# Kernel optimization log

Hardware: AMD Instinct MI355X
Metric: run time of the kernel (lower is better)

Reference implementation:

```python
import jax, jax.numpy as jnp
import numpy as np

# ---- geometry constants (match init_kwargs) ----
A = 24            # standardAngleNum
U, V = 128, 64    # detectorSize = [U, V]
W, H, D = 128, 128, 64  # volumeSize = [W, H, D]
SID, SDD = 256.0, 512.0
S = 128           # samples per ray
HS = 100.0        # half-span of ray sampling around isocenter (covers volume half-diagonal ~96)
STEP = 2.0 * HS / S
ANGLES = np.deg2rad(np.linspace(0.0, 360.0, A, False)).astype(np.float32)
LAMB = 1.0


def _cos_weight():
    # cosine[..., i, j] = SDD / sqrt(SDD^2 + (i - V/2)^2 + (j - U/2)^2), i over V, j over U
    i = np.arange(V)[:, None].astype(np.float64)
    j = np.arange(U)[None, :].astype(np.float64)
    w = SDD / np.sqrt(SDD ** 2 + (i - V / 2.0) ** 2 + (j - U / 2.0) ** 2)
    return jnp.asarray(w[None, None, None], jnp.float32)  # [1,1,1,V,U], broadcasts over A


def _ramp():
    # Ram-Lak spatial-domain filter, length U+1, OIHW kernel [1,1,1,U+1]
    i = np.arange(U + 1, dtype=np.float64)
    mid = np.floor(U / 2.0)
    d = i - mid
    f = np.where(d % 2 == 0, 0.0, -0.5 / (np.pi ** 2 * np.where(d == 0, 1.0, d * d)))
    f[int(mid)] = 0.125  # 1/8 at center
    return jnp.asarray(f.reshape(1, 1, 1, U + 1), jnp.float32)


COSW = _cos_weight()
RAMP = _ramp()


def forward_project(vol):
    """Ray-driven cone-beam forward projection. vol: [D,H,W] -> sino [A,V,U]. Linear in vol."""
    uu = jnp.arange(U, dtype=jnp.float32) - (U - 1) / 2.0
    vv = jnp.arange(V, dtype=jnp.float32) - (V - 1) / 2.0
    ell = jnp.linspace(SID - HS, SID + HS, S, dtype=jnp.float32)  # distance from source

    def body(_, cs):
        c, s = cs
        z = jnp.zeros_like(c)
        src = jnp.stack([-SID * c, -SID * s, z])                 # source position [3]
        dc = jnp.stack([(SDD - SID) * c, (SDD - SID) * s, z])    # detector center [3]
        uax = jnp.stack([-s, c, z])                              # detector u axis
        vax = jnp.array([0.0, 0.0, 1.0], jnp.float32)            # detector v axis
        pix = dc + uu[None, :, None] * uax + vv[:, None, None] * vax  # [V,U,3]
        dirs = pix - src
        dirs = dirs / jnp.linalg.norm(dirs, axis=-1, keepdims=True)   # unit ray dirs [V,U,3]
        pts = src + ell[:, None, None, None] * dirs[None]             # [S,V,U,3]
        coords = [pts[..., 2] + (D - 1) / 2.0,   # z -> depth index
                  pts[..., 1] + (H - 1) / 2.0,   # y -> row index
                  pts[..., 0] + (W - 1) / 2.0]   # x -> col index
        vals = jax.scipy.ndimage.map_coordinates(vol, coords, order=1, mode='constant', cval=0.0)
        return None, vals.sum(axis=0) * STEP     # [V,U]

    ang = jnp.asarray(ANGLES)
    _, sino = jax.lax.scan(body, None, (jnp.cos(ang), jnp.sin(ang)))
    return sino  # [A,V,U]


def back_project(sino):
    """Exact adjoint of forward_project (matches projector.forward/backward adjoint pair)."""
    _, vjp = jax.vjp(forward_project, jnp.zeros((D, H, W), jnp.float32))
    (vol,) = vjp(sino)
    return vol


def fbp(x, p):
    # residual = FP(x) - p
    sino = forward_project(x[0, 0])[None, None]       # [1,1,A,V,U]
    res = (sino - p) * COSW                           # cosine weighting
    # ramp filtering along detector u, done as conv2d on [b,c,A*V,U]
    r2 = res.reshape(1, 1, A * V, U)
    r2 = jax.lax.conv_general_dilated(r2, RAMP, (1, 1), ((0, 0), (U // 2, U // 2)),
                                      dimension_numbers=('NCHW', 'OIHW', 'NCHW'))
    res = r2.reshape(1, 1, A, V, U)
    return LAMB * back_project(res[0, 0])[None, None]  # [1,1,D,H,W]


def setup_inputs() -> dict:
    key = jax.random.key(0)
    k1, k2 = jax.random.split(key)
    x = jax.random.normal(k1, (1, 1, D, H, W), jnp.float32)
    p = jax.random.normal(k2, (1, 1, A, V, U), jnp.float32)
    return {"x": x, "p": p}


def reference(x, p):
    return fbp(x, p)
```

## Files before the change

kernel.cpp:

```cpp
#include <hip/hip_runtime.h>
#include <math.h>

#define NA   24
#define NU   128
#define NV   64
#define NW   128
#define NH   128
#define ND   64
#define NS   128
#define F_STEP 1.5625f
#define F_DL  (200.0f / 127.0f)
#define F_L0  156.0f
#define INV_DL (127.0f / 200.0f)

#define NRAYS (NA * NV * NU)
#define VOX   (NW * NH * ND)
#define NSEG  4

#define PPX  130
#define PPY  130
#define PPZ  68
#define PPLANE (PPX * PPY)
#define PVN  (PPZ * PPLANE)
#define CBASE (2 * PPLANE + PPX + 1)

typedef float v2f __attribute__((ext_vector_type(2)));

__device__ __constant__ float CSA[NA] = {
    1.0f,  0.96592582628906829f,  0.86602540378443865f,  0.70710678118654752f,
    0.5f,  0.25881904510252076f,  0.0f,                 -0.25881904510252076f,
   -0.5f, -0.70710678118654752f, -0.86602540378443865f, -0.96592582628906829f,
   -1.0f, -0.96592582628906829f, -0.86602540378443865f, -0.70710678118654752f,
   -0.5f, -0.25881904510252076f,  0.0f,                  0.25881904510252076f,
    0.5f,  0.70710678118654752f,  0.86602540378443865f,  0.96592582628906829f
};
__device__ __constant__ float SNA[NA] = {
    0.0f,  0.25881904510252076f,  0.5f,                  0.70710678118654752f,
    0.86602540378443865f,  0.96592582628906829f,  1.0f,  0.96592582628906829f,
    0.86602540378443865f,  0.70710678118654752f,  0.5f,  0.25881904510252076f,
    0.0f, -0.25881904510252076f, -0.5f,                 -0.70710678118654752f,
   -0.86602540378443865f, -0.96592582628906829f, -1.0f, -0.96592582628906829f,
   -0.86602540378443865f, -0.70710678118654752f, -0.5f, -0.25881904510252076f
};

__global__ __launch_bounds__(256) void pad_kernel(const float* __restrict__ vol,
                                                  float* __restrict__ padv) {
    int i = blockIdx.x * 256 + threadIdx.x;
    if (i >= PVN) return;
    int x = i % PPX;
    int t = i / PPX;
    int y = t % PPY;
    int z = t / PPY;
    float val = 0.0f;
    if (z >= 2 && z <= 65 && y >= 1 && y <= 128 && x >= 1 && x <= 128)
        val = vol[(((z - 2) << 7) + (y - 1) << 7) + (x - 1)];
    padv[i] = val;
}

__device__ __forceinline__ void ray_setup(int a, int v, int u,
                                          float& sx, float& sy,
                                          float& dx, float& dy, float& dz) {
    float ang = (float)((double)a * (15.0 * M_PI / 180.0));
    float c = cosf(ang), s = sinf(ang);
    float uu = (float)u - 63.5f;
    float vv = (float)v - 31.5f;
    float ux = 512.0f * c - uu * s;
    float uy = 512.0f * s + uu * c;
    float uz = vv;
    float invn = 1.0f / sqrtf(ux * ux + uy * uy + uz * uz);
    dx = ux * invn; dy = uy * invn; dz = uz * invn;
    sx = -256.0f * c; sy = -256.0f * s;
}

__global__ __launch_bounds__(256) void fp_seg_kernel(const float* __restrict__ padv,
                                                     float* __restrict__ part) {
    int r = blockIdx.x * blockDim.x + threadIdx.x;
    int seg = blockIdx.y;
    int u = r & (NU - 1);
    int v = (r >> 7) & (NV - 1);
    int a = r >> 13;

    float sx, sy, dx, dy, dz;
    ray_setup(a, v, u, sx, sy, dx, dy, dz);

    float rx = 1.0f / dx, ry = 1.0f / dy, rz = 1.0f / dz;
    float ex0 = (-64.51f - sx) * rx, ex1 = (64.51f - sx) * rx;
    float ey0 = (-64.51f - sy) * ry, ey1 = (64.51f - sy) * ry;
    float ez0 = (-32.51f) * rz,      ez1 = (32.51f) * rz;
    float llo = fmaxf(fmaxf(fminf(ex0, ex1), fminf(ey0, ey1)), fminf(ez0, ez1));
    float lhi = fminf(fminf(fmaxf(ex0, ex1), fmaxf(ey0, ey1)), fmaxf(ez0, ez1));
    int i_lo = max(seg * 32,      (int)ceilf((llo - F_L0) * INV_DL));
    int i_hi = min(seg * 32 + 31, (int)floorf((lhi - F_L0) * INV_DL));

    float acc = 0.0f;
    for (int i = i_lo; i <= i_hi; ++i) {
        float ell = fmaf((float)i, F_DL, F_L0);
        float cx = fmaf(ell, dx, sx) + 63.5f;
        float cy = fmaf(ell, dy, sy) + 63.5f;
        float cz = ell * dz + 31.5f;
        float fx = floorf(cx), fy = floorf(cy), fz = floorf(cz);
        int ix = (int)fx, iy = (int)fy, iz = (int)fz;
        float wx1 = cx - fx, wy1 = cy - fy, wz1 = cz - fz;
        int base = iz * PPLANE + iy * PPX + ix + CBASE;
        const float* q0 = padv + base;
        const float* q1 = q0 + PPLANE;
        float v000 = q0[0],   v001 = q0[1];
        float v010 = q0[PPX], v011 = q0[PPX + 1];
        float v100 = q1[0],   v101 = q1[1];
        float v110 = q1[PPX], v111 = q1[PPX + 1];
        float c00 = fmaf(wx1, v001 - v000, v000);
        float c01 = fmaf(wx1, v011 - v010, v010);
        float c10 = fmaf(wx1, v101 - v100, v100);
        float c11 = fmaf(wx1, v111 - v110, v110);
        float c0  = fmaf(wy1, c01 - c00, c00);
        float c1  = fmaf(wy1, c11 - c10, c10);
        acc += fmaf(wz1, c1 - c0, c0);
    }
    part[seg * NRAYS + r] = acc;
}

__global__ __launch_bounds__(NU) void ramp_kernel(const float* __restrict__ part,
                                                  const float* __restrict__ p,
                                                  float* __restrict__ resT) {
    __shared__ float row[NU];
    int rowid = blockIdx.x;
    int u = threadIdx.x;
    int e = rowid * NU + u;
    int a = rowid >> 6;
    int v = rowid & (NV - 1);
    float sino = (part[e] + part[NRAYS + e] + part[2 * NRAYS + e] + part[3 * NRAYS + e]) * F_STEP;
    double du = (double)u - 64.0;
    double dv = (double)v - 32.0;
    float cw = (float)(512.0 / sqrt(262144.0 + dv * dv + du * du));
    row[u] = (sino - p[e]) * cw;
    __syncthreads();
    float acc = 0.125f * row[u];
#pragma unroll
    for (int d = 1; d <= 63; d += 2) {
        float f = (float)(-0.5 / (M_PI * M_PI * (double)(d * d)));
        float lo = (u - d >= 0) ? row[u - d] : 0.0f;
        float hi = (u + d < NU) ? row[u + d] : 0.0f;
        acc += f * (lo + hi);
    }
    resT[(a << 13) + (u << 6) + v] = acc;
}


#define SETUP_ANGLE(S, AIDX, AB)                                                 \
    const float c##S = CSA[AIDX], sn##S = SNA[AIDX];                             \
    const float c512##S = 512.0f * c##S;                                         \
    const float s512##S = 512.0f * sn##S;                                        \
    const float rho##S = fmaf(x0, c##S, fmaf(y0, sn##S, 256.0f));                \
    const float Vx##S = x0 + 256.0f * c##S;                                      \
    const float Vy##S = y0 + 256.0f * sn##S;                                     \
    const float tvlo##S = (rho##S - (AB)) * (1.0f / 512.0f);                     \
    const float yp##S = y0 * c##S - x0 * sn##S;                                  \
    const float rl##S = __builtin_amdgcn_rcpf(rho##S - (AB));                    \
    const float rh##S = __builtin_amdgcn_rcpf(rho##S + (AB));                    \
    const float A##S = yp##S - (AB), B##S = yp##S + (AB);                        \
    const float um##S = 512.0f * A##S * ((A##S >= 0.0f) ? rh##S : rl##S);        \
    const float uM##S = 512.0f * B##S * ((B##S >= 0.0f) ? rl##S : rh##S);        \
    const int u_lo##S = max(0,   (int)ceilf(um##S + 63.49f));                    \
    const int u_hi##S = min(127, (int)floorf(uM##S + 63.51f));                   \
    const int len##S = max(0, u_hi##S - u_lo##S + 1);                            \
    const float Zmin##S = fmaf(vvf, (vvf >= 0.0f) ? (tvlo##S - 1.0e-3f)          \
                                                  : (tvlo##S + 7.2e-3f), 31.5f); \
    const float izbf##S = floorf(Zmin##S);                                       \
    const int   izb##S  = (int)izbf##S;                                          \
    const v2f b0##S = {izbf##S, izbf##S};                                        \
    const float tDL##S = tvlo##S * INV_DL;                                       \
    const v2f mVx##S = {-Vx##S, -Vx##S}, mVy##S = {-Vy##S, -Vy##S};

#define BP_BODY2(S, RV, UU) do {                                                 \
    const float pu = fmaf(-(UU), sn##S, c512##S);                                \
    const float qu = fmaf((UU), c##S, s512##S);                                  \
    const float arg  = fmaf((UU), (UU), s2);                                     \
    const float invn = __builtin_amdgcn_rsqf(arg);                               \
    const float nn   = arg * invn;                                               \
    const float i0f  = ceilf(fmaf(tDL##S, nn, cK));                              \
    const float ell0 = fmaf(i0f, F_DL, F_L0);                                    \
    v2f tp; tp.x = ell0 * invn; tp.y = fmaf(F_DL, invn, tp.x);                   \
    const v2f pu2 = {pu, pu}, qu2 = {qu, qu};                                    \
    v2f wx = __builtin_elementwise_max(                                          \
        one2 - __builtin_elementwise_abs(__builtin_elementwise_fma(tp, pu2, mVx##S)), zero2); \
    v2f wy = __builtin_elementwise_max(                                          \
        one2 - __builtin_elementwise_abs(__builtin_elementwise_fma(tp, qu2, mVy##S)), zero2); \
    v2f val = wx * wy * (v2f){(RV), (RV)};                                       \
    const v2f fz2 = __builtin_elementwise_fma(tp, vv2, h31);                     \
    const v2f g = fz2 - b0##S;                                                   \
    AC0##S = __builtin_elementwise_fma(__builtin_elementwise_max(                \
             one2 - __builtin_elementwise_abs(g), zero2), val, AC0##S);          \
    AC1##S = __builtin_elementwise_fma(__builtin_elementwise_max(                \
             one2 - __builtin_elementwise_abs(g - one2), zero2), val, AC1##S);   \
    AC2##S = __builtin_elementwise_fma(__builtin_elementwise_max(                \
             one2 - __builtin_elementwise_abs(g - two2), zero2), val, AC2##S);   \
} while (0)

__global__ __launch_bounds__(256, 8) void bp_gather14(const float* __restrict__ resT,
                                                      float* __restrict__ out) {
    __shared__ float s_acc[4 * 64];

    const int tid  = threadIdx.x;
    const int lane = tid & 63;
    const int wv   = tid >> 6;
    const int y    = blockIdx.x & 127;
    const int xq   = blockIdx.x >> 7;
    const int xi   = xq * 4 + wv;

    const float x0 = (float)xi - 63.5f;
    const float y0 = (float)y  - 63.5f;
    const float vvf = (float)lane - 31.5f;
    const float s2  = fmaf(vvf, vvf, 262144.0f);
    const v2f vv2   = {vvf, vvf};
    const v2f one2  = {1.0f, 1.0f}, zero2 = {0.0f, 0.0f};
    const v2f two2  = {2.0f, 2.0f};
    const v2f h31   = {31.5f, 31.5f};
    const float cK  = -(F_L0 * INV_DL) - 1.0e-3f;

    s_acc[tid] = 0.0f;

    for (int j = 0; j < NA / 2; ++j) {
        const int a0 = 2 * j, a1 = 2 * j + 1;
        const float ab1a = fabsf(CSA[a0]) + fabsf(SNA[a0]);
        const float ab1b = fabsf(CSA[a1]) + fabsf(SNA[a1]);

        SETUP_ANGLE(0, a0, ab1a);
        SETUP_ANGLE(1, a1, ab1b);

        const int trips = (max(len0, len1) + 1) & ~1;
        if (trips == 0) continue;
        const int us0 = max(0, min(u_lo0, 128 - trips));
        const int us1 = max(0, min(u_lo1, 128 - trips));

        v2f AC00 = zero2, AC10 = zero2, AC20 = zero2;
        v2f AC01 = zero2, AC11 = zero2, AC21 = zero2;

        const float* ru0 = resT + (a0 << 13) + (us0 << 6) + lane;
        const float* ru1 = resT + (a1 << 13) + (us1 << 6) + lane;
        float uu0 = (float)us0 - 63.5f;
        float uu1 = (float)us1 - 63.5f;

        float Ar0 = ru0[0],  Ar1 = ru1[0];
        float Br0 = ru0[64], Br1 = ru1[64];
#pragma unroll 1
        for (int k = 0; k < trips; k += 2) {
            const float Cr0 = ru0[128];
            const float Cr1 = ru1[128];
            const float Dr0 = ru0[192];
            const float Dr1 = ru1[192];
            BP_BODY2(0, Ar0, uu0);
            BP_BODY2(1, Ar1, uu1);
            BP_BODY2(0, Br0, uu0 + 1.0f);
            BP_BODY2(1, Br1, uu1 + 1.0f);
            Ar0 = Cr0; Ar1 = Cr1; Br0 = Dr0; Br1 = Dr1;
            ru0 += 128; ru1 += 128;
            uu0 += 2.0f; uu1 += 2.0f;
        }

        float* accw = s_acc + (wv << 6);
        atomicAdd(&accw[izb0],     AC00.x + AC00.y);
        atomicAdd(&accw[izb0 + 1], AC10.x + AC10.y);
        atomicAdd(&accw[izb0 + 2], AC20.x + AC20.y);
        atomicAdd(&accw[izb1],     AC01.x + AC01.y);
        atomicAdd(&accw[izb1 + 1], AC11.x + AC11.y);
        atomicAdd(&accw[izb1 + 2], AC21.x + AC21.y);
    }
    __syncthreads();

    const int z  = tid >> 2;
    const int w4 = tid & 3;
    out[(z << 14) + (y << 7) + xq * 4 + w4] = s_acc[(w4 << 6) + z] * F_STEP;
}

extern "C" void kernel_launch(void* const* d_in, const int* in_sizes, int n_in,
                              void* d_out, int out_size, void* d_ws, size_t ws_size,
                              hipStream_t stream) {
    const float* x = (const float*)d_in[0];
    const float* p = (const float*)d_in[1];
    float* out  = (float*)d_out;
    float* resT = (float*)d_ws;
    float* part = resT + NRAYS;
    float* padv = part + NSEG * NRAYS;

    pad_kernel<<<(PVN + 255) / 256, 256, 0, stream>>>(x, padv);
    dim3 fpg(NRAYS / 256, NSEG);
    fp_seg_kernel<<<fpg, 256, 0, stream>>>(padv, part);
    ramp_kernel<<<NA * NV, NU, 0, stream>>>(part, p, resT);
    bp_gather14<<<128 * 32, 256, 0, stream>>>(resT, out);
}
```

Baseline: 431.3 us.

## Software-pipeline angle-pair setup and first loads in backprojection gather

Computes the geometry and issues the first two residual loads for the next angle pair before processing the current pair, so setup latency and load latency overlap the inner accumulation loop. It also simplifies the third z-weight to max(g-2+1,0) form (max(h1,0)) and relaxes launch bounds from 8 to 4 blocks per SM, giving more registers at the cost of potential occupancy. The zero-trip early skip is removed, and the last iteration prefetches pair 0 redundantly.

```diff
diff --git a/kernel.cpp b/kernel.cpp
--- a/kernel.cpp
+++ b/kernel.cpp
@@ -146,57 +146,73 @@
 }
 
 
-#define SETUP_ANGLE(S, AIDX, AB)                                                 \
-    const float c##S = CSA[AIDX], sn##S = SNA[AIDX];                             \
-    const float c512##S = 512.0f * c##S;                                         \
-    const float s512##S = 512.0f * sn##S;                                        \
-    const float rho##S = fmaf(x0, c##S, fmaf(y0, sn##S, 256.0f));                \
-    const float Vx##S = x0 + 256.0f * c##S;                                      \
-    const float Vy##S = y0 + 256.0f * sn##S;                                     \
-    const float tvlo##S = (rho##S - (AB)) * (1.0f / 512.0f);                     \
-    const float yp##S = y0 * c##S - x0 * sn##S;                                  \
-    const float rl##S = __builtin_amdgcn_rcpf(rho##S - (AB));                    \
-    const float rh##S = __builtin_amdgcn_rcpf(rho##S + (AB));                    \
-    const float A##S = yp##S - (AB), B##S = yp##S + (AB);                        \
-    const float um##S = 512.0f * A##S * ((A##S >= 0.0f) ? rh##S : rl##S);        \
-    const float uM##S = 512.0f * B##S * ((B##S >= 0.0f) ? rl##S : rh##S);        \
-    const int u_lo##S = max(0,   (int)ceilf(um##S + 63.49f));                    \
-    const int u_hi##S = min(127, (int)floorf(uM##S + 63.51f));                   \
-    const int len##S = max(0, u_hi##S - u_lo##S + 1);                            \
-    const float Zmin##S = fmaf(vvf, (vvf >= 0.0f) ? (tvlo##S - 1.0e-3f)          \
-                                                  : (tvlo##S + 7.2e-3f), 31.5f); \
-    const float izbf##S = floorf(Zmin##S);                                       \
-    const int   izb##S  = (int)izbf##S;                                          \
-    const v2f b0##S = {izbf##S, izbf##S};                                        \
-    const float tDL##S = tvlo##S * INV_DL;                                       \
-    const v2f mVx##S = {-Vx##S, -Vx##S}, mVy##S = {-Vy##S, -Vy##S};
+#define DECL_ANG(P) \
+    float P##_c, P##_sn, P##_tDL, P##_izbf; \
+    int P##_ulo, P##_len, P##_us; \
+    float P##_Ar, P##_Br;
+
+#define COPY_ANG(D, S) do { \
+    D##_c = S##_c; D##_sn = S##_sn; D##_tDL = S##_tDL; D##_izbf = S##_izbf; \
+    D##_us = S##_us; D##_Ar = S##_Ar; D##_Br = S##_Br; \
+} while (0)
+
+#define SETUP_P(P, AIDX) do { \
+    const float c_ = CSA[(AIDX)], s_ = SNA[(AIDX)]; \
+    const float ab_ = fabsf(c_) + fabsf(s_); \
+    const float rho_ = fmaf(x0, c_, fmaf(y0, s_, 256.0f)); \
+    const float tvlo_ = (rho_ - ab_) * (1.0f / 512.0f); \
+    const float yp_ = y0 * c_ - x0 * s_; \
+    const float rl_ = __builtin_amdgcn_rcpf(rho_ - ab_); \
+    const float rh_ = __builtin_amdgcn_rcpf(rho_ + ab_); \
+    const float A_ = yp_ - ab_, B_ = yp_ + ab_; \
+    const float um_ = 512.0f * A_ * ((A_ >= 0.0f) ? rh_ : rl_); \
+    const float uM_ = 512.0f * B_ * ((B_ >= 0.0f) ? rl_ : rh_); \
+    P##_ulo = max(0, (int)ceilf(um_ + 63.49f)); \
+    P##_len = min(127, (int)floorf(uM_ + 63.51f)) - P##_ulo + 1; \
+    const float zm_ = fmaf(vvf, (vvf >= 0.0f) ? (tvlo_ - 1.0e-3f) \
+                                              : (tvlo_ + 7.2e-3f), 31.5f); \
+    P##_izbf = floorf(zm_); \
+    P##_tDL  = tvlo_ * INV_DL; \
+    P##_c = c_; P##_sn = s_; \
+} while (0)
+
+#define PAIR_FINISH(P0, P1, TR) do { \
+    TR = (max(max(P0##_len, P1##_len), 0) + 1) & ~1; \
+    P0##_us = max(0, min(P0##_ulo, 128 - TR)); \
+    P1##_us = max(0, min(P1##_ulo, 128 - TR)); \
+} while (0)
+
+#define ISSUE(P, AIDX) do { \
+    const float* r_ = resT + ((AIDX) << 13) + (P##_us << 6) + lane; \
+    P##_Ar = r_[0]; P##_Br = r_[64]; \
+} while (0)
 
 #define BP_BODY2(S, RV, UU) do {                                                 \
-    const float pu = fmaf(-(UU), sn##S, c512##S);                                \
-    const float qu = fmaf((UU), c##S, s512##S);                                  \
+    const float pu = fmaf(-(UU), ksn##S, kc512##S);                              \
+    const float qu = fmaf((UU), kc##S, ks512##S);                                \
     const float arg  = fmaf((UU), (UU), s2);                                     \
     const float invn = __builtin_amdgcn_rsqf(arg);                               \
     const float nn   = arg * invn;                                               \
-    const float i0f  = ceilf(fmaf(tDL##S, nn, cK));                              \
+    const float i0f  = ceilf(fmaf(ktDL##S, nn, cK));                             \
     const float ell0 = fmaf(i0f, F_DL, F_L0);                                    \
     v2f tp; tp.x = ell0 * invn; tp.y = fmaf(F_DL, invn, tp.x);                   \
     const v2f pu2 = {pu, pu}, qu2 = {qu, qu};                                    \
     v2f wx = __builtin_elementwise_max(                                          \
-        one2 - __builtin_elementwise_abs(__builtin_elementwise_fma(tp, pu2, mVx##S)), zero2); \
+        one2 - __builtin_elementwise_abs(__builtin_elementwise_fma(tp, pu2, kmVx##S)), zero2); \
     v2f wy = __builtin_elementwise_max(                                          \
-        one2 - __builtin_elementwise_abs(__builtin_elementwise_fma(tp, qu2, mVy##S)), zero2); \
+        one2 - __builtin_elementwise_abs(__builtin_elementwise_fma(tp, qu2, kmVy##S)), zero2); \
     v2f val = wx * wy * (v2f){(RV), (RV)};                                       \
     const v2f fz2 = __builtin_elementwise_fma(tp, vv2, h31);                     \
-    const v2f g = fz2 - b0##S;                                                   \
+    const v2f g  = fz2 - kb0##S;                                                 \
+    const v2f h1 = g - one2;                                                     \
     AC0##S = __builtin_elementwise_fma(__builtin_elementwise_max(                \
              one2 - __builtin_elementwise_abs(g), zero2), val, AC0##S);          \
     AC1##S = __builtin_elementwise_fma(__builtin_elementwise_max(                \
-             one2 - __builtin_elementwise_abs(g - one2), zero2), val, AC1##S);   \
-    AC2##S = __builtin_elementwise_fma(__builtin_elementwise_max(                \
-             one2 - __builtin_elementwise_abs(g - two2), zero2), val, AC2##S);   \
-} while (0)
-
-__global__ __launch_bounds__(256, 8) void bp_gather14(const float* __restrict__ resT,
+             one2 - __builtin_elementwise_abs(h1), zero2), val, AC1##S);         \
+    AC2##S = __builtin_elementwise_fma(__builtin_elementwise_max(h1, zero2), val, AC2##S); \
+} while (0)
+
+__global__ __launch_bounds__(256, 4) void bp_gather15(const float* __restrict__ resT,
                                                       float* __restrict__ out) {
     __shared__ float s_acc[4 * 64];
 
@@ -213,37 +229,52 @@
     const float s2  = fmaf(vvf, vvf, 262144.0f);
     const v2f vv2   = {vvf, vvf};
     const v2f one2  = {1.0f, 1.0f}, zero2 = {0.0f, 0.0f};
-    const v2f two2  = {2.0f, 2.0f};
     const v2f h31   = {31.5f, 31.5f};
     const float cK  = -(F_L0 * INV_DL) - 1.0e-3f;
 
     s_acc[tid] = 0.0f;
 
+    DECL_ANG(C0); DECL_ANG(C1); DECL_ANG(N0); DECL_ANG(N1);
+    int cur_trips, nxt_trips;
+
+    SETUP_P(C0, 0); SETUP_P(C1, 1);
+    PAIR_FINISH(C0, C1, cur_trips);
+    ISSUE(C0, 0); ISSUE(C1, 1);
+
     for (int j = 0; j < NA / 2; ++j) {
-        const int a0 = 2 * j, a1 = 2 * j + 1;
-        const float ab1a = fabsf(CSA[a0]) + fabsf(SNA[a0]);
-        const float ab1b = fabsf(CSA[a1]) + fabsf(SNA[a1]);
-
-        SETUP_ANGLE(0, a0, ab1a);
-        SETUP_ANGLE(1, a1, ab1b);
-
-        const int trips = (max(len0, len1) + 1) & ~1;
-        if (trips == 0) continue;
-        const int us0 = max(0, min(u_lo0, 128 - trips));
-        const int us1 = max(0, min(u_lo1, 128 - trips));
+        const int a0 = 2 * j, a1 = a0 + 1;
+
+        const int jn = (j + 1 < NA / 2) ? (j + 1) : 0;
+        SETUP_P(N0, 2 * jn); SETUP_P(N1, 2 * jn + 1);
+        PAIR_FINISH(N0, N1, nxt_trips);
+        ISSUE(N0, 2 * jn); ISSUE(N1, 2 * jn + 1);
+
+        const float kc0 = C0_c, ksn0 = C0_sn;
+        const float kc1 = C1_c, ksn1 = C1_sn;
+        const float kc5120 = 512.0f * kc0, ks5120 = 512.0f * ksn0;
+        const float kc5121 = 512.0f * kc1, ks5121 = 512.0f * ksn1;
+        const float mvx0 = fmaf(-256.0f, kc0, -x0);
+        const float mvy0 = fmaf(-256.0f, ksn0, -y0);
+        const float mvx1 = fmaf(-256.0f, kc1, -x0);
+        const float mvy1 = fmaf(-256.0f, ksn1, -y0);
+        const v2f kmVx0 = {mvx0, mvx0}, kmVy0 = {mvy0, mvy0};
+        const v2f kmVx1 = {mvx1, mvx1}, kmVy1 = {mvy1, mvy1};
+        const float ktDL0 = C0_tDL, ktDL1 = C1_tDL;
+        const v2f kb00 = {C0_izbf, C0_izbf};
+        const v2f kb01 = {C1_izbf, C1_izbf};
 
         v2f AC00 = zero2, AC10 = zero2, AC20 = zero2;
         v2f AC01 = zero2, AC11 = zero2, AC21 = zero2;
 
-        const float* ru0 = resT + (a0 << 13) + (us0 << 6) + lane;
-        const float* ru1 = resT + (a1 << 13) + (us1 << 6) + lane;
-        float uu0 = (float)us0 - 63.5f;
-        float uu1 = (float)us1 - 63.5f;
-
-        float Ar0 = ru0[0],  Ar1 = ru1[0];
-        float Br0 = ru0[64], Br1 = ru1[64];
+        const float* ru0 = resT + (a0 << 13) + (C0_us << 6) + lane;
+        const float* ru1 = resT + (a1 << 13) + (C1_us << 6) + lane;
+        float uu0 = (float)C0_us - 63.5f;
+        float uu1 = (float)C1_us - 63.5f;
+
+        float Ar0 = C0_Ar, Ar1 = C1_Ar;
+        float Br0 = C0_Br, Br1 = C1_Br;
 #pragma unroll 1
-        for (int k = 0; k < trips; k += 2) {
+        for (int k = 0; k < cur_trips; k += 2) {
             const float Cr0 = ru0[128];
             const float Cr1 = ru1[128];
             const float Dr0 = ru0[192];
@@ -258,12 +289,17 @@
         }
 
         float* accw = s_acc + (wv << 6);
+        const int izb0 = (int)C0_izbf;
+        const int izb1 = (int)C1_izbf;
         atomicAdd(&accw[izb0],     AC00.x + AC00.y);
         atomicAdd(&accw[izb0 + 1], AC10.x + AC10.y);
         atomicAdd(&accw[izb0 + 2], AC20.x + AC20.y);
         atomicAdd(&accw[izb1],     AC01.x + AC01.y);
         atomicAdd(&accw[izb1 + 1], AC11.x + AC11.y);
         atomicAdd(&accw[izb1 + 2], AC21.x + AC21.y);
+
+        COPY_ANG(C0, N0); COPY_ANG(C1, N1);
+        cur_trips = nxt_trips;
     }
     __syncthreads();
 
@@ -286,5 +322,5 @@
     dim3 fpg(NRAYS / 256, NSEG);
     fp_seg_kernel<<<fpg, 256, 0, stream>>>(padv, part);
     ramp_kernel<<<NA * NV, NU, 0, stream>>>(part, p, resT);
-    bp_gather14<<<128 * 32, 256, 0, stream>>>(resT, out);
-}
+    bp_gather15<<<128 * 32, 256, 0, stream>>>(resT, out);
+}
```

Result: slower. 562.1 us (+30.3%).
